# Kernel optimization log

Measured on AMD Instinct MI355X. Metric: run time of the kernel, lower is better.

The kernel has to match this reference:

```python
import jax, jax.numpy as jnp
import numpy as np

DIM = 1024
HEADS = 16
HEAD_DIM = DIM // HEADS
SCALE = HEAD_DIM ** -0.5


def setup_inputs() -> dict:
    key = jax.random.key(0)
    k1, k2, k3, k4 = jax.random.split(key, 4)
    x = jax.random.normal(k1, (2, 2048, DIM), dtype=jnp.float32)
    # nn.Linear(dim, 3*dim, bias=False): weight shape (3*dim, dim), y = x @ W.T
    w_qkv = jax.random.normal(k2, (3 * DIM, DIM), dtype=jnp.float32) * (DIM ** -0.5)
    w_proj = jax.random.normal(k3, (DIM, DIM), dtype=jnp.float32) * (DIM ** -0.5)
    head_w = jnp.ones((HEADS,), dtype=jnp.float32)
    return {"x": x, "w_qkv": w_qkv, "w_proj": w_proj, "head_w": head_w}


def reference(x, w_qkv, w_proj, head_w) -> jnp.ndarray:
    B, N, C = x.shape
    qkv = jnp.einsum("bnc,dc->bnd", x, w_qkv)  # [B,N,3C]
    qkv = qkv.reshape(B, N, 3, HEADS, HEAD_DIM).transpose(2, 0, 3, 1, 4)
    q, k, v = qkv[0], qkv[1], qkv[2]  # each [B,H,N,Dh]
    attn = jnp.einsum("bhqd,bhkd->bhqk", q, k) * SCALE  # [B,H,N,N]
    attn = jax.nn.softmax(attn, axis=-1)
    out = jnp.einsum("bhqk,bhkd->bhqd", attn, v)  # [B,H,N,Dh]
    hw = jax.nn.softmax(head_w)[None, :, None, None]
    out = out * hw
    out = out.transpose(0, 2, 1, 3).reshape(B, N, C)
    return jnp.einsum("bnc,dc->bnd", out, w_proj)
```

## Files before the change

kernel.cpp:

```cpp
#include <hip/hip_runtime.h>

typedef _Float16 half_t;
typedef _Float16 half8 __attribute__((ext_vector_type(8)));
typedef _Float16 half4_t __attribute__((ext_vector_type(4)));
typedef float floatx4 __attribute__((ext_vector_type(4)));
typedef float floatx16 __attribute__((ext_vector_type(16)));

#define B_SZ 2
#define SEQ 2048
#define DIM_ 1024
#define NH 16
#define DH 64
#define ROWS (B_SZ * SEQ)

__device__ __forceinline__ void gl2lds16(const void* g, void* l) {
  __builtin_amdgcn_global_load_lds((const __attribute__((address_space(1))) unsigned int*)g,
                                   (__attribute__((address_space(3))) unsigned int*)l, 16, 0, 0);
}

__global__ __launch_bounds__(256) void convert_all(const float4* __restrict__ x,
                                                   const float4* __restrict__ wq,
                                                   const float4* __restrict__ wp,
                                                   half4_t* __restrict__ dst,
                                                   int nx, int nq, int np) {
  int i = blockIdx.x * blockDim.x + threadIdx.x;
  float4 v;
  if (i < nx) v = x[i];
  else if (i < nx + nq) v = wq[i - nx];
  else if (i < nx + nq + np) v = wp[i - nx - nq];
  else return;
  half4_t h;
  h.x = (half_t)v.x; h.y = (half_t)v.y; h.z = (half_t)v.z; h.w = (half_t)v.w;
  dst[i] = h;
}

template <int MODE, int BN>
__global__ __launch_bounds__(256, 3) void gemm32(const half_t* __restrict__ A,
                                                 const half_t* __restrict__ Bt,
                                                 half_t* __restrict__ q16,
                                                 half_t* __restrict__ k16,
                                                 half_t* __restrict__ vT16,
                                                 float* __restrict__ outp) {
  constexpr int K = 1024;
  constexpr int BK = 32;
  constexpr int NT = BN / 64;
  __shared__ __align__(16) half_t a_lds[2][128 * BK];
  __shared__ __align__(16) half_t b_lds[2][BN * BK];
  const int t = threadIdx.x;
  const int wave = t >> 6, lane = t & 63;
  const int l31 = lane & 31, hw = lane >> 5;
  const int wm = wave >> 1, wn = wave & 1;
  const int row0 = blockIdx.y * 128, col0 = blockIdx.x * BN;

  floatx16 acc[2][NT];
#pragma unroll
  for (int i = 0; i < 2; ++i)
#pragma unroll
    for (int j = 0; j < NT; ++j)
#pragma unroll
      for (int r = 0; r < 16; ++r) acc[i][j][r] = 0.f;

  auto stage = [&](int buf, int k0) {
#pragma unroll
    for (int hi = 0; hi < 2; ++hi) {
      int s = t + hi * 256;
      int row = ((s >> 3) << 1) | (s & 1);
      int c = (s >> 1) & 3;
      int sc = c ^ ((row >> 2) & 3);
      gl2lds16(A + (size_t)(row0 + row) * K + (k0 + sc * 8),
               &a_lds[buf][(wave * 64 + hi * 256) * 8]);
    }
#pragma unroll
    for (int hi = 0; hi < BN / 64; ++hi) {
      int s = t + hi * 256;
      int row = ((s >> 3) << 1) | (s & 1);
      int c = (s >> 1) & 3;
      int sc = c ^ ((row >> 2) & 3);
      gl2lds16(Bt + (size_t)(col0 + row) * K + (k0 + sc * 8),
               &b_lds[buf][(wave * 64 + hi * 256) * 8]);
    }
  };

  stage(0, 0);
  int cur = 0;
  for (int k0 = 0; k0 < K; k0 += BK) {
    __syncthreads();
    if (k0 + BK < K) stage(cur ^ 1, k0 + BK);

#pragma unroll
    for (int kf = 0; kf < 2; ++kf) {
      half8 af[2], bf[NT];
#pragma unroll
      for (int mt = 0; mt < 2; ++mt) {
        int row = wm * 64 + mt * 32 + l31;
        int c_lds = ((kf << 1) | hw) ^ ((row >> 2) & 3);
        af[mt] = *(const half8*)(&a_lds[cur][(row >> 1) * 64 + c_lds * 16 + (row & 1) * 8]);
      }
#pragma unroll
      for (int nt = 0; nt < NT; ++nt) {
        int row = wn * (BN / 2) + nt * 32 + l31;
        int c_lds = ((kf << 1) | hw) ^ ((row >> 2) & 3);
        bf[nt] = *(const half8*)(&b_lds[cur][(row >> 1) * 64 + c_lds * 16 + (row & 1) * 8]);
      }
#pragma unroll
      for (int mt = 0; mt < 2; ++mt)
#pragma unroll
        for (int nt = 0; nt < NT; ++nt)
          acc[mt][nt] = __builtin_amdgcn_mfma_f32_32x32x16_f16(af[mt], bf[nt], acc[mt][nt], 0, 0, 0);
    }
    cur ^= 1;
  }

  if (MODE == 0) {
    const int which = col0 >> 10;
#pragma unroll
    for (int mt = 0; mt < 2; ++mt)
#pragma unroll
      for (int nt = 0; nt < NT; ++nt) {
        int growb = row0 + wm * 64 + mt * 32;
        int gcol = col0 + wn * (BN / 2) + nt * 32 + l31;
        int hc = gcol & 1023, h = hc >> 6, d = hc & 63;
        if (which == 2) {
#pragma unroll
          for (int rq = 0; rq < 4; ++rq) {
            int grow = growb + 8 * rq + 4 * hw;
            int b = grow >> 11, n0 = grow & 2047;
            int bh = b * NH + h;
            half4_t h4;
            h4.x = (half_t)acc[mt][nt][rq * 4 + 0];
            h4.y = (half_t)acc[mt][nt][rq * 4 + 1];
            h4.z = (half_t)acc[mt][nt][rq * 4 + 2];
            h4.w = (half_t)acc[mt][nt][rq * 4 + 3];
            *(half4_t*)(vT16 + ((size_t)bh * DH + d) * SEQ + n0) = h4;
          }
        } else {
#pragma unroll
          for (int r = 0; r < 16; ++r) {
            int grow = growb + (r & 3) + 8 * (r >> 2) + 4 * hw;
            int b = grow >> 11, n = grow & 2047;
            int bh = b * NH + h;
            float v = acc[mt][nt][r];
            if (which == 0)
              q16[((size_t)bh * SEQ + n) * DH + d] = (half_t)(v * 0.18033688011112042f);
            else
              k16[((size_t)bh * SEQ + n) * DH + d] = (half_t)v;
          }
        }
      }
  } else {
#pragma unroll
    for (int mt = 0; mt < 2; ++mt)
#pragma unroll
      for (int nt = 0; nt < NT; ++nt) {
        int growb = row0 + wm * 64 + mt * 32;
        int gcol = col0 + wn * (BN / 2) + nt * 32 + l31;
#pragma unroll
        for (int r = 0; r < 16; ++r) {
          int grow = growb + (r & 3) + 8 * (r >> 2) + 4 * hw;
          outp[(size_t)grow * DIM_ + gcol] = acc[mt][nt][r];
        }
      }
  }
}

__global__ __launch_bounds__(256, 4) void attn_p1(const half_t* __restrict__ q16,
                                                  const half_t* __restrict__ k16,
                                                  const half_t* __restrict__ vT16,
                                                  half_t* __restrict__ opart,
                                                  float* __restrict__ psums) {
  __shared__ __align__(16) half_t k_lds[2][64 * 64];
  __shared__ __align__(16) half_t v_lds[2][64 * 64];

  const int t = threadIdx.x;
  const int wave = t >> 6, lane = t & 63;
  const int l15 = lane & 15, quad = lane >> 4;
  const int blk = blockIdx.x;
  const int js = blk & 1, qt = (blk >> 1) & 15, bh = blk >> 5;
  const half_t* qp = q16 + (size_t)bh * SEQ * DH;
  const half_t* kp = k16 + (size_t)bh * SEQ * DH;
  const half_t* vp = vT16 + (size_t)bh * DH * SEQ;
  const int q0w = qt * 128 + wave * 32;
  const int jbase = js * 1024;

  const int s0 = t, s1 = t + 256;
  const int r0_ = s0 >> 3, c0_ = (s0 & 7) ^ (r0_ & 7);
  const int r1_ = s1 >> 3, c1_ = (s1 & 7) ^ (r1_ & 7);

  half8 qf[2][2];
#pragma unroll
  for (int mi = 0; mi < 2; ++mi)
#pragma unroll
    for (int kf = 0; kf < 2; ++kf)
      qf[mi][kf] = *(const half8*)(qp + (size_t)(q0w + mi * 16 + l15) * DH + kf * 32 + quad * 8);

  const floatx4 z4 = {0.f, 0.f, 0.f, 0.f};
  floatx4 o[2][4];
  floatx4 osum[2];
#pragma unroll
  for (int mi = 0; mi < 2; ++mi) {
    osum[mi] = z4;
#pragma unroll
    for (int i = 0; i < 4; ++i) o[mi][i] = z4;
  }

  gl2lds16(kp + (size_t)(jbase + r0_) * DH + c0_ * 8, &k_lds[0][(wave * 64) * 8]);
  gl2lds16(vp + (size_t)r0_ * SEQ + jbase + c0_ * 8, &v_lds[0][(wave * 64) * 8]);
  gl2lds16(kp + (size_t)(jbase + r1_) * DH + c1_ * 8, &k_lds[0][(wave * 64 + 256) * 8]);
  gl2lds16(vp + (size_t)r1_ * SEQ + jbase + c1_ * 8, &v_lds[0][(wave * 64 + 256) * 8]);

  const half_t one_h = (half_t)1.f;
  const half4_t vone = {one_h, one_h, one_h, one_h};

  int cur = 0;
  for (int jt = 0; jt < 16; ++jt) {
    __syncthreads();

    if (jt + 1 < 16) {
      const int j0 = jbase + (jt + 1) * 64, nb = cur ^ 1;
      gl2lds16(kp + (size_t)(j0 + r0_) * DH + c0_ * 8, &k_lds[nb][(wave * 64) * 8]);
      gl2lds16(vp + (size_t)r0_ * SEQ + j0 + c0_ * 8, &v_lds[nb][(wave * 64) * 8]);
      gl2lds16(kp + (size_t)(j0 + r1_) * DH + c1_ * 8, &k_lds[nb][(wave * 64 + 256) * 8]);
      gl2lds16(vp + (size_t)r1_ * SEQ + j0 + c1_ * 8, &v_lds[nb][(wave * 64 + 256) * 8]);
    }

    const half_t* kl = k_lds[cur];
    const half_t* vl = v_lds[cur];

    half4_t pf[2][4];
#pragma unroll
    for (int nt = 0; nt < 4; ++nt) {
      int row = nt * 16 + l15;
      floatx4 st0 = z4, st1 = z4;
#pragma unroll
      for (int kf = 0; kf < 2; ++kf) {
        half8 kb = *(const half8*)(kl + row * 64 + (((kf << 2) | quad) ^ (row & 7)) * 8);
        st0 = __builtin_amdgcn_mfma_f32_16x16x32_f16(kb, qf[0][kf], st0, 0, 0, 0);
        st1 = __builtin_amdgcn_mfma_f32_16x16x32_f16(kb, qf[1][kf], st1, 0, 0, 0);
      }
      {
        half4_t pk;
        pk.x = (half_t)__builtin_amdgcn_exp2f(st0[0]);
        pk.y = (half_t)__builtin_amdgcn_exp2f(st0[1]);
        pk.z = (half_t)__builtin_amdgcn_exp2f(st0[2]);
        pk.w = (half_t)__builtin_amdgcn_exp2f(st0[3]);
        pf[0][nt] = pk;
      }
      {
        half4_t pk;
        pk.x = (half_t)__builtin_amdgcn_exp2f(st1[0]);
        pk.y = (half_t)__builtin_amdgcn_exp2f(st1[1]);
        pk.z = (half_t)__builtin_amdgcn_exp2f(st1[2]);
        pk.w = (half_t)__builtin_amdgcn_exp2f(st1[3]);
        pf[1][nt] = pk;
      }
    }

#pragma unroll
    for (int jt2 = 0; jt2 < 4; ++jt2) {
#pragma unroll
      for (int dt = 0; dt < 4; ++dt) {
        int row = dt * 16 + l15;
        int ch = (jt2 * 2 + (quad >> 1)) ^ (l15 & 7);
        half4_t vb = *(const half4_t*)(vl + row * 64 + ch * 8 + (quad & 1) * 4);
        o[0][dt] = __builtin_amdgcn_mfma_f32_16x16x16f16(pf[0][jt2], vb, o[0][dt], 0, 0, 0);
        o[1][dt] = __builtin_amdgcn_mfma_f32_16x16x16f16(pf[1][jt2], vb, o[1][dt], 0, 0, 0);
      }
      osum[0] = __builtin_amdgcn_mfma_f32_16x16x16f16(pf[0][jt2], vone, osum[0], 0, 0, 0);
      osum[1] = __builtin_amdgcn_mfma_f32_16x16x16f16(pf[1][jt2], vone, osum[1], 0, 0, 0);
    }
    cur ^= 1;
  }

  if (l15 == 0) {
#pragma unroll
    for (int mi = 0; mi < 2; ++mi)
#pragma unroll
      for (int r = 0; r < 4; ++r)
        psums[((size_t)(js * 32 + bh)) * SEQ + q0w + mi * 16 + quad * 4 + r] = osum[mi][r];
  }

#pragma unroll
  for (int mi = 0; mi < 2; ++mi)
#pragma unroll
    for (int r = 0; r < 4; ++r) {
      int n = q0w + mi * 16 + quad * 4 + r;
      size_t base = ((size_t)(js * 32 + bh) * SEQ + n) * DH;
#pragma unroll
      for (int dt = 0; dt < 4; ++dt)
        opart[base + dt * 16 + l15] = (half_t)o[mi][dt][r];
    }
}

__global__ __launch_bounds__(256) void combine(const half_t* __restrict__ opart,
                                               const float* __restrict__ psums,
                                               const float* __restrict__ head_w,
                                               half_t* __restrict__ attn16) {
  int idx = blockIdx.x * blockDim.x + threadIdx.x;
  int d4 = idx & 15, n = (idx >> 4) & 2047, bh = idx >> 15;
  int h = bh & 15, b = bh >> 4;
  const size_t jstr = (size_t)32 * SEQ * DH;
  size_t off = ((size_t)bh * SEQ + n) * DH + d4 * 4;
  half4_t o0 = *(const half4_t*)(opart + off);
  half4_t o1 = *(const half4_t*)(opart + jstr + off);
  float ps = psums[(size_t)bh * SEQ + n] + psums[(size_t)32 * SEQ + (size_t)bh * SEQ + n];

  float mw = head_w[0];
#pragma unroll
  for (int i = 1; i < NH; ++i) mw = fmaxf(mw, head_w[i]);
  float sw = 0.f;
#pragma unroll
  for (int i = 0; i < NH; ++i) sw += __expf(head_w[i] - mw);
  float hwv = __expf(head_w[h] - mw) / sw;

  float scl = hwv / ps;
  half4_t r;
  r.x = (half_t)(((float)o0.x + (float)o1.x) * scl);
  r.y = (half_t)(((float)o0.y + (float)o1.y) * scl);
  r.z = (half_t)(((float)o0.z + (float)o1.z) * scl);
  r.w = (half_t)(((float)o0.w + (float)o1.w) * scl);
  *(half4_t*)(attn16 + ((size_t)(b * SEQ + n)) * DIM_ + h * DH + d4 * 4) = r;
}

extern "C" void kernel_launch(void* const* d_in, const int* in_sizes, int n_in,
                              void* d_out, int out_size, void* d_ws, size_t ws_size,
                              hipStream_t stream) {
  const float* x = (const float*)d_in[0];
  const float* w_qkv = (const float*)d_in[1];
  const float* w_proj = (const float*)d_in[2];
  const float* head_w = (const float*)d_in[3];
  float* out = (float*)d_out;

  half_t* x16 = (half_t*)d_ws;
  half_t* wq16 = x16 + (size_t)ROWS * DIM_;
  half_t* wp16 = wq16 + (size_t)3 * DIM_ * DIM_;
  half_t* q16 = wp16 + (size_t)DIM_ * DIM_;
  half_t* k16 = q16 + (size_t)ROWS * DIM_;
  half_t* vT16 = k16 + (size_t)ROWS * DIM_;
  half_t* attn16 = vT16 + (size_t)ROWS * DIM_;
  half_t* opart = attn16 + (size_t)ROWS * DIM_;
  float* psums = (float*)(opart + (size_t)2 * 32 * SEQ * DH);

  const int nx = ROWS * DIM_ / 4, nq = 3 * DIM_ * DIM_ / 4, np = DIM_ * DIM_ / 4;
  convert_all<<<(nx + nq + np) / 256, 256, 0, stream>>>((const float4*)x, (const float4*)w_qkv,
                                                        (const float4*)w_proj, (half4_t*)x16,
                                                        nx, nq, np);

  gemm32<0, 128><<<dim3(24, 32), 256, 0, stream>>>(x16, wq16, q16, k16, vT16, nullptr);
  attn_p1<<<32 * 16 * 2, 256, 0, stream>>>(q16, k16, vT16, opart, psums);
  combine<<<(32 * SEQ * DH / 4) / 256, 256, 0, stream>>>(opart, psums, head_w, attn16);
  gemm32<1, 64><<<dim3(16, 32), 256, 0, stream>>>(attn16, wp16, nullptr, nullptr, nullptr, out);
}
```

Baseline: 200.6 us.

## Stage GEMM tiles through registers instead of direct global-to-LDS loads

Replaces the double-buffered direct global_load_lds staging with register prefetch: the next K-tile is loaded into registers while the current single-buffered LDS tile is consumed, then written to LDS at the top of the next iteration. This halves LDS usage, which may allow higher occupancy, and uses a simpler row-major XOR swizzle. It adds a second __syncthreads per iteration, extra VGPR pressure for the prefetch registers, and explicit ds_write instructions.

Result: faster. 193.5 us (-3.5%).

```diff
diff --git a/kernel.cpp b/kernel.cpp
--- a/kernel.cpp
+++ b/kernel.cpp
@@ -44,14 +44,30 @@
   constexpr int K = 1024;
   constexpr int BK = 32;
   constexpr int NT = BN / 64;
-  __shared__ __align__(16) half_t a_lds[2][128 * BK];
-  __shared__ __align__(16) half_t b_lds[2][BN * BK];
+  constexpr int NB = BN / 64;
+  __shared__ __align__(16) half_t a_lds[128 * BK];
+  __shared__ __align__(16) half_t b_lds[BN * BK];
   const int t = threadIdx.x;
   const int wave = t >> 6, lane = t & 63;
   const int l31 = lane & 31, hw = lane >> 5;
   const int wm = wave >> 1, wn = wave & 1;
   const int row0 = blockIdx.y * 128, col0 = blockIdx.x * BN;
 
+  int rowA[2], scA[2];
+#pragma unroll
+  for (int hi = 0; hi < 2; ++hi) {
+    int s = t + hi * 256;
+    rowA[hi] = s >> 2;
+    scA[hi] = (s & 3) ^ ((rowA[hi] >> 1) & 3);
+  }
+  int rowB[NB], scB[NB];
+#pragma unroll
+  for (int hi = 0; hi < NB; ++hi) {
+    int s = t + hi * 256;
+    rowB[hi] = s >> 2;
+    scB[hi] = (s & 3) ^ ((rowB[hi] >> 1) & 3);
+  }
+
   floatx16 acc[2][NT];
 #pragma unroll
   for (int i = 0; i < 2; ++i)
@@ -60,32 +76,29 @@
 #pragma unroll
       for (int r = 0; r < 16; ++r) acc[i][j][r] = 0.f;
 
-  auto stage = [&](int buf, int k0) {
-#pragma unroll
-    for (int hi = 0; hi < 2; ++hi) {
-      int s = t + hi * 256;
-      int row = ((s >> 3) << 1) | (s & 1);
-      int c = (s >> 1) & 3;
-      int sc = c ^ ((row >> 2) & 3);
-      gl2lds16(A + (size_t)(row0 + row) * K + (k0 + sc * 8),
-               &a_lds[buf][(wave * 64 + hi * 256) * 8]);
-    }
-#pragma unroll
-    for (int hi = 0; hi < BN / 64; ++hi) {
-      int s = t + hi * 256;
-      int row = ((s >> 3) << 1) | (s & 1);
-      int c = (s >> 1) & 3;
-      int sc = c ^ ((row >> 2) & 3);
-      gl2lds16(Bt + (size_t)(col0 + row) * K + (k0 + sc * 8),
-               &b_lds[buf][(wave * 64 + hi * 256) * 8]);
-    }
+  half8 sa[2][2], sb[2][NB];
+
+  auto loadT = [&](int pp, int k0) {
+#pragma unroll
+    for (int hi = 0; hi < 2; ++hi)
+      sa[pp][hi] = *(const half8*)(A + (size_t)(row0 + rowA[hi]) * K + (k0 + scA[hi] * 8));
+#pragma unroll
+    for (int hi = 0; hi < NB; ++hi)
+      sb[pp][hi] = *(const half8*)(Bt + (size_t)(col0 + rowB[hi]) * K + (k0 + scB[hi] * 8));
   };
 
-  stage(0, 0);
-  int cur = 0;
+  loadT(0, 0);
+  int pp = 0;
   for (int k0 = 0; k0 < K; k0 += BK) {
+#pragma unroll
+    for (int hi = 0; hi < 2; ++hi)
+      *(half8*)(&a_lds[(t + hi * 256) * 8]) = sa[pp][hi];
+#pragma unroll
+    for (int hi = 0; hi < NB; ++hi)
+      *(half8*)(&b_lds[(t + hi * 256) * 8]) = sb[pp][hi];
     __syncthreads();
-    if (k0 + BK < K) stage(cur ^ 1, k0 + BK);
+
+    if (k0 + BK < K) loadT(pp ^ 1, k0 + BK);
 
 #pragma unroll
     for (int kf = 0; kf < 2; ++kf) {
@@ -93,14 +106,12 @@
 #pragma unroll
       for (int mt = 0; mt < 2; ++mt) {
         int row = wm * 64 + mt * 32 + l31;
-        int c_lds = ((kf << 1) | hw) ^ ((row >> 2) & 3);
-        af[mt] = *(const half8*)(&a_lds[cur][(row >> 1) * 64 + c_lds * 16 + (row & 1) * 8]);
+        af[mt] = *(const half8*)(&a_lds[row * BK + (((kf << 1) | hw) ^ ((row >> 1) & 3)) * 8]);
       }
 #pragma unroll
       for (int nt = 0; nt < NT; ++nt) {
         int row = wn * (BN / 2) + nt * 32 + l31;
-        int c_lds = ((kf << 1) | hw) ^ ((row >> 2) & 3);
-        bf[nt] = *(const half8*)(&b_lds[cur][(row >> 1) * 64 + c_lds * 16 + (row & 1) * 8]);
+        bf[nt] = *(const half8*)(&b_lds[row * BK + (((kf << 1) | hw) ^ ((row >> 1) & 3)) * 8]);
       }
 #pragma unroll
       for (int mt = 0; mt < 2; ++mt)
@@ -108,7 +119,8 @@
         for (int nt = 0; nt < NT; ++nt)
           acc[mt][nt] = __builtin_amdgcn_mfma_f32_32x32x16_f16(af[mt], bf[nt], acc[mt][nt], 0, 0, 0);
     }
-    cur ^= 1;
+    __syncthreads();
+    pp ^= 1;
   }
 
   if (MODE == 0) {
```
